# Kernel optimization log

Hardware: AMD Instinct MI355X
Metric: run time of the kernel (lower is better)

## Reference

```python
import jax, jax.numpy as jnp
import numpy as np

WCNT = 100000; EMB = 300; T = 256; S = 256; K = 10; L = 128; N = 8192


def gru_cell(x, h, wih, whh, bih, bhh):
    # torch GRU cell: gates ordered (r, z, n)
    gi = x @ wih.T + bih
    gh = h @ whh.T + bhh
    ir, iz, inn = jnp.split(gi, 3, axis=-1)
    hr, hz, hn = jnp.split(gh, 3, axis=-1)
    r = jax.nn.sigmoid(ir + hr)
    z = jax.nn.sigmoid(iz + hz)
    n = jnp.tanh(inn + r * hn)
    return (1.0 - z) * n + z * h


def gru_scan(xs, h0, wih, whh, bih, bhh):
    def step(h, x):
        hn = gru_cell(x, h, wih, whh, bih, bhh)
        return hn, hn
    _, ys = jax.lax.scan(step, h0, xs)
    return ys


def setup_inputs() -> dict:
    key = jax.random.key(0)
    ks = jax.random.split(key, 30)
    def rn(k, shape, scale=0.05):
        return jax.random.normal(k, shape, dtype=jnp.float32) * scale
    inp = {}
    inp["topic"] = jax.random.randint(ks[0], (L,), 0, WCNT)
    inp["score"] = jax.random.uniform(ks[1], (1,), dtype=jnp.float32)
    inp["time"] = jax.random.uniform(ks[2], (1,), dtype=jnp.float32)
    inp["h"] = rn(ks[3], (1, 1, S), 1.0)
    inp["vs"] = rn(ks[4], (N, T), 1.0)
    inp["hs"] = rn(ks[5], (N, 1, S), 1.0)
    inp["emb"] = rn(ks[6], (WCNT, EMB), 1.0)
    # word-level bidirectional GRU (input EMB, hidden T)
    inp["w_ih_f"] = rn(ks[7], (3 * T, EMB)); inp["w_hh_f"] = rn(ks[8], (3 * T, T))
    inp["b_ih_f"] = rn(ks[9], (3 * T,));     inp["b_hh_f"] = rn(ks[10], (3 * T,))
    inp["w_ih_b"] = rn(ks[11], (3 * T, EMB)); inp["w_hh_b"] = rn(ks[12], (3 * T, T))
    inp["b_ih_b"] = rn(ks[13], (3 * T,));     inp["b_hh_b"] = rn(ks[14], (3 * T,))
    # output GRU (input 2T, hidden T)
    inp["w_ih_o"] = rn(ks[15], (3 * T, 2 * T)); inp["w_hh_o"] = rn(ks[16], (3 * T, T))
    inp["b_ih_o"] = rn(ks[17], (3 * T,));       inp["b_hh_o"] = rn(ks[18], (3 * T,))
    # sequence GRU step (input 2T+1 for score_mode='double', hidden S)
    inp["w_ih_s"] = rn(ks[19], (3 * S, 2 * T + 1)); inp["w_hh_s"] = rn(ks[20], (3 * S, S))
    inp["b_ih_s"] = rn(ks[21], (3 * S,));           inp["b_hh_s"] = rn(ks[22], (3 * S,))
    # score head: in_features = topic_size + (2*S + 1) since with_last=True
    inp["score_w"] = rn(ks[23], (1, T + 2 * S + 1)); inp["score_b"] = rn(ks[24], (1,))
    return inp


def reference(topic, score, time, h, vs, hs, emb,
              w_ih_f, w_hh_f, b_ih_f, b_hh_f,
              w_ih_b, w_hh_b, b_ih_b, b_hh_b,
              w_ih_o, w_hh_o, b_ih_o, b_hh_o,
              w_ih_s, w_hh_s, b_ih_s, b_hh_s,
              score_w, score_b):
    # ---- TopicRNNModel (batch 1, batch dim dropped) ----
    x = emb[topic]                                  # [L, EMB]
    z0 = jnp.zeros((T,), dtype=x.dtype)
    yf = gru_scan(x, z0, w_ih_f, w_hh_f, b_ih_f, b_hh_f)          # [L, T]
    yb = gru_scan(x[::-1], z0, w_ih_b, w_hh_b, b_ih_b, b_hh_b)[::-1]
    y = jnp.concatenate([yf, yb], axis=-1)          # [L, 2T]
    v = gru_scan(y, z0, w_ih_o, w_hh_o, b_ih_o, b_hh_o)[-1]       # [T] = topic_v[0]
    # ---- AttnSeqModel: top-k attention over past hidden states ----
    alpha = vs @ v                                  # [N]
    a, idx = jax.lax.top_k(alpha, K)
    w = jax.nn.softmax(a)                           # [K]
    attn_h = w @ hs.reshape(-1, S)[idx]             # [S]
    length = jnp.full((1,), float(K), dtype=v.dtype)
    pred_v = jnp.concatenate([v, attn_h, h.reshape(-1), length])  # [T+2S+1]
    sc = (pred_v @ score_w.T + score_b).reshape(1, 1)
    # ---- GRU step (score_mode='double') ----
    gp = (score >= 0.5).astype(v.dtype)
    gn = (score < 0.5).astype(v.dtype)
    x_in = jnp.concatenate([v * gp, v * gn, score])  # [2T+1]
    h_new = gru_cell(x_in, h.reshape(-1), w_ih_s, w_hh_s, b_ih_s, b_hh_s).reshape(1, 1, S)
    # ---- updated history caches ----
    vs_new = jnp.concatenate([vs, v[None]], axis=0)
    hs_new = jnp.concatenate([hs, h_new], axis=0)
    return sc, h_new, vs_new, hs_new
```

## Files before the change

kernel.cpp:

```cpp
#include <hip/hip_runtime.h>
#include <cfloat>

#define EMB 300
#define TT 256
#define SS 256
#define KK 10
#define LL 128
#define NN 8192
#define G3 768

typedef _Float16 half2_t __attribute__((ext_vector_type(2)));

#if __has_builtin(__builtin_amdgcn_fdot2)
#define FDOT2(a, b, c) __builtin_amdgcn_fdot2((a), (b), (c), false)
#else
#define FDOT2(a, b, c) ((c) + (float)(a).x * (float)(b).x + (float)(a).y * (float)(b).y)
#endif

__device__ __forceinline__ float sigmoidf_(float x) {
    return __builtin_amdgcn_rcpf(1.0f + __expf(-x));
}
__device__ __forceinline__ float tanhf_(float x) {
    return 2.0f * __builtin_amdgcn_rcpf(1.0f + __expf(-2.0f * x)) - 1.0f;
}

__global__ void k_input_gates_word(const int* __restrict__ topic, const float* __restrict__ emb,
                                   const float* __restrict__ wihF, const float* __restrict__ bihF,
                                   const float* __restrict__ wihB, const float* __restrict__ bihB,
                                   float* __restrict__ giF, float* __restrict__ giB) {
    __shared__ float4 xl[EMB / 4];
    const int l = blockIdx.x;
    const int dir = blockIdx.y;
    const float* wih = dir ? wihB : wihF;
    const float* bih = dir ? bihB : bihF;
    float* gi = dir ? giB : giF;
    const int word = topic[l];
    const float4* xrow = (const float4*)(emb + (size_t)word * EMB);
    if (threadIdx.x < EMB / 4) xl[threadIdx.x] = xrow[threadIdx.x];
    __syncthreads();
    const int j = threadIdx.x;
    const float4* wr = (const float4*)(wih + (size_t)j * EMB);
    float acc = bih[j];
    #pragma unroll 5
    for (int c = 0; c < EMB / 4; ++c) {
        float4 w4 = wr[c], x4 = xl[c];
        acc += w4.x * x4.x + w4.y * x4.y + w4.z * x4.z + w4.w * x4.w;
    }
    gi[l * G3 + j] = acc;
}

__global__ void k_input_gates_out(const float* __restrict__ yF, const float* __restrict__ yB,
                                  const float* __restrict__ wihO, const float* __restrict__ bihO,
                                  float* __restrict__ giO) {
    __shared__ float4 yl[128];
    const int l = blockIdx.x;
    if (threadIdx.x < 64) {
        yl[threadIdx.x] = ((const float4*)(yF + l * TT))[threadIdx.x];
        yl[64 + threadIdx.x] = ((const float4*)(yB + l * TT))[threadIdx.x];
    }
    __syncthreads();
    const int j = threadIdx.x;
    const float4* wr = (const float4*)(wihO + (size_t)j * 512);
    float acc = bihO[j];
    #pragma unroll 4
    for (int c = 0; c < 128; ++c) {
        float4 w4 = wr[c], x4 = yl[c];
        acc += w4.x * x4.x + w4.y * x4.y + w4.z * x4.z + w4.w * x4.w;
    }
    giO[l * G3 + j] = acc;
}

__launch_bounds__(512, 2)
__global__ void k_gru_scan(const float* __restrict__ giA, const float* __restrict__ whhA,
                           const float* __restrict__ bhhA, float* __restrict__ yA, int revA,
                           const float* __restrict__ giB_, const float* __restrict__ whhB,
                           const float* __restrict__ bhhB, float* __restrict__ yB_, int revB) {
    const float* gi; const float* whh; const float* bhh; float* y; int rev;
    if (blockIdx.x == 0) { gi = giA; whh = whhA; bhh = bhhA; y = yA; rev = revA; }
    else                 { gi = giB_; whh = whhB; bhh = bhhB; y = yB_; rev = revB; }

    __shared__ __align__(16) unsigned int h_u32[TT / 2];
    __shared__ float part1[G3];
    __shared__ float gh_lds[G3];

    const int tid = threadIdx.x;
    const int grp = tid >> 8;
    const int r3 = tid & 255;
    const int row0 = r3 * 3;
    const int koff = grp * 128;

    half2_t w[3][64];
    float bias[3];
    #pragma unroll
    for (int rr = 0; rr < 3; ++rr) {
        const float4* wrow4 = (const float4*)(whh + (size_t)(row0 + rr) * TT + koff);
        #pragma unroll
        for (int q = 0; q < 32; ++q) {
            float4 f = wrow4[q];
            half2_t t0; t0.x = (_Float16)f.x; t0.y = (_Float16)f.y;
            half2_t t1; t1.x = (_Float16)f.z; t1.y = (_Float16)f.w;
            w[rr][2 * q] = t0;
            w[rr][2 * q + 1] = t1;
        }
        bias[rr] = (grp == 0) ? bhh[row0 + rr] : 0.0f;
    }

    for (int i = tid; i < TT / 2; i += blockDim.x) h_u32[i] = 0u;
    float hcur = 0.0f;
    __syncthreads();

    for (int t = 0; t < LL; ++t) {
        const int idx = rev ? (LL - 1 - t) : t;
        float gir = 0.f, giz = 0.f, gin = 0.f;
        if (grp == 0) {
            gir = gi[idx * G3 + r3];
            giz = gi[idx * G3 + 256 + r3];
            gin = gi[idx * G3 + 512 + r3];
        }
        float acc0 = bias[0], acc1 = bias[1], acc2 = bias[2];
        const uint4* h4 = (const uint4*)h_u32;
        #pragma unroll
        for (int c = 0; c < 16; ++c) {
            uint4 hu = h4[grp * 16 + c];
            half2_t hq0 = __builtin_bit_cast(half2_t, hu.x);
            half2_t hq1 = __builtin_bit_cast(half2_t, hu.y);
            half2_t hq2 = __builtin_bit_cast(half2_t, hu.z);
            half2_t hq3 = __builtin_bit_cast(half2_t, hu.w);
            acc0 = FDOT2(w[0][c * 4 + 0], hq0, acc0);
            acc1 = FDOT2(w[1][c * 4 + 0], hq0, acc1);
            acc2 = FDOT2(w[2][c * 4 + 0], hq0, acc2);
            acc0 = FDOT2(w[0][c * 4 + 1], hq1, acc0);
            acc1 = FDOT2(w[1][c * 4 + 1], hq1, acc1);
            acc2 = FDOT2(w[2][c * 4 + 1], hq1, acc2);
            acc0 = FDOT2(w[0][c * 4 + 2], hq2, acc0);
            acc1 = FDOT2(w[1][c * 4 + 2], hq2, acc1);
            acc2 = FDOT2(w[2][c * 4 + 2], hq2, acc2);
            acc0 = FDOT2(w[0][c * 4 + 3], hq3, acc0);
            acc1 = FDOT2(w[1][c * 4 + 3], hq3, acc1);
            acc2 = FDOT2(w[2][c * 4 + 3], hq3, acc2);
        }
        if (grp == 1) {
            part1[row0] = acc0; part1[row0 + 1] = acc1; part1[row0 + 2] = acc2;
        }
        __syncthreads();
        if (grp == 0) {
            gh_lds[row0]     = acc0 + part1[row0];
            gh_lds[row0 + 1] = acc1 + part1[row0 + 1];
            gh_lds[row0 + 2] = acc2 + part1[row0 + 2];
        }
        __syncthreads();
        if (grp == 0) {
            const int i = r3;
            float r = sigmoidf_(gir + gh_lds[i]);
            float z = sigmoidf_(giz + gh_lds[256 + i]);
            float n = tanhf_(gin + r * gh_lds[512 + i]);
            hcur = (1.0f - z) * n + z * hcur;
            y[idx * TT + i] = hcur;
            ((_Float16*)h_u32)[i] = (_Float16)hcur;
        }
        __syncthreads();
    }
}

__global__ void k_alpha(const float* __restrict__ vs, const float* __restrict__ v,
                        float* __restrict__ alpha) {
    const int wv = threadIdx.x >> 6;
    const int lane = threadIdx.x & 63;
    const int n = blockIdx.x * 4 + wv;
    float4 a = ((const float4*)(vs + (size_t)n * TT))[lane];
    float4 b = ((const float4*)v)[lane];
    float p = a.x * b.x + a.y * b.y + a.z * b.z + a.w * b.w;
    #pragma unroll
    for (int off = 32; off; off >>= 1) p += __shfl_down(p, off, 64);
    if (lane == 0) alpha[n] = p;
}

__global__ void k_gates_s(const float* __restrict__ v, const float* __restrict__ score,
                          const float* __restrict__ hin,
                          const float* __restrict__ wihS, const float* __restrict__ bihS,
                          const float* __restrict__ whhS, const float* __restrict__ bhhS,
                          float* __restrict__ gis, float* __restrict__ ghs) {
    const int j = blockIdx.x * blockDim.x + threadIdx.x;
    if (j >= G3) return;
    const float sc = score[0];
    const float gp = (sc >= 0.5f) ? 1.0f : 0.0f;
    const float gn = 1.0f - gp;
    const float* wi = wihS + (size_t)j * (2 * TT + 1);
    float a = bihS[j];
    for (int c = 0; c < TT; ++c) a += wi[c] * (v[c] * gp);
    for (int c = 0; c < TT; ++c) a += wi[TT + c] * (v[c] * gn);
    a += wi[2 * TT] * sc;
    gis[j] = a;
    const float* wh = whhS + (size_t)j * SS;
    float g = bhhS[j];
    for (int c = 0; c < SS; ++c) g += wh[c] * hin[c];
    ghs[j] = g;
}

__global__ void k_head(const float* __restrict__ alpha_g, const float* __restrict__ v,
                       const float* __restrict__ hin, const float* __restrict__ hs,
                       const float* __restrict__ score_w, const float* __restrict__ score_b,
                       const float* __restrict__ gis, const float* __restrict__ ghs,
                       float* __restrict__ d_out, float* __restrict__ hnew_ws) {
    __shared__ float sa[NN];
    __shared__ float wbv[16];
    __shared__ int wbi[16];
    __shared__ float topv[KK];
    __shared__ int topi[KK];
    __shared__ float wk[KK];
    __shared__ float predv[G3 + 8];
    const int tid = threadIdx.x;
    for (int i = tid; i < NN; i += 1024) sa[i] = alpha_g[i];
    __syncthreads();
    for (int it = 0; it < KK; ++it) {
        float bv = -FLT_MAX; int bi = 0x7fffffff;
        #pragma unroll
        for (int k = 0; k < 8; ++k) {
            int i = tid + 1024 * k;
            float x = sa[i];
            if (x > bv) { bv = x; bi = i; }
        }
        #pragma unroll
        for (int off = 32; off; off >>= 1) {
            float ov = __shfl_down(bv, off, 64);
            int oi = __shfl_down(bi, off, 64);
            if (ov > bv || (ov == bv && oi < bi)) { bv = ov; bi = oi; }
        }
        const int lane = tid & 63, wv = tid >> 6;
        if (lane == 0) { wbv[wv] = bv; wbi[wv] = bi; }
        __syncthreads();
        if (tid == 0) {
            float Bv = wbv[0]; int Bi = wbi[0];
            for (int wq = 1; wq < 16; ++wq)
                if (wbv[wq] > Bv || (wbv[wq] == Bv && wbi[wq] < Bi)) { Bv = wbv[wq]; Bi = wbi[wq]; }
            topv[it] = Bv; topi[it] = Bi;
            sa[Bi] = -FLT_MAX;
        }
        __syncthreads();
    }
    if (tid == 0) {
        float m = topv[0], s = 0.0f, e[KK];
        for (int k = 0; k < KK; ++k) { e[k] = __expf(topv[k] - m); s += e[k]; }
        float rs = 1.0f / s;
        for (int k = 0; k < KK; ++k) wk[k] = e[k] * rs;
    }
    __syncthreads();
    if (tid < TT) {
        float ah = 0.0f;
        #pragma unroll
        for (int k = 0; k < KK; ++k) ah += wk[k] * hs[(size_t)topi[k] * SS + tid];
        predv[tid] = v[tid];
        predv[TT + tid] = ah;
        predv[2 * TT + tid] = hin[tid];
        if (tid == 0) predv[G3] = (float)KK;
    }
    __syncthreads();
    if (tid < 64) {
        float p = 0.0f;
        for (int c = tid; c < G3 + 1; c += 64) p += predv[c] * score_w[c];
        #pragma unroll
        for (int off = 32; off; off >>= 1) p += __shfl_down(p, off, 64);
        if (tid == 0) d_out[0] = p + score_b[0];
    }
    if (tid < SS) {
        const int i = tid;
        float r = sigmoidf_(gis[i] + ghs[i]);
        float z = sigmoidf_(gis[TT + i] + ghs[TT + i]);
        float n = tanhf_(gis[2 * TT + i] + r * ghs[2 * TT + i]);
        float hn = (1.0f - z) * n + z * hin[i];
        d_out[1 + i] = hn;
        hnew_ws[i] = hn;
    }
}

__global__ void k_finalize(const float* __restrict__ vs, const float* __restrict__ hs,
                           const float* __restrict__ v, const float* __restrict__ hnew,
                           float* __restrict__ d_out) {
    const size_t i = (size_t)blockIdx.x * blockDim.x + threadIdx.x;
    const size_t stride = (size_t)gridDim.x * blockDim.x;
    float* vs_out = d_out + 1 + TT;
    float* hs_out = vs_out + (size_t)(NN + 1) * TT;
    for (size_t x = i; x < (size_t)NN * TT; x += stride) vs_out[x] = vs[x];
    for (size_t x = i; x < (size_t)NN * SS; x += stride) hs_out[x] = hs[x];
    if (i < TT) vs_out[(size_t)NN * TT + i] = v[i];
    if (i < SS) hs_out[(size_t)NN * SS + i] = hnew[i];
}

extern "C" void kernel_launch(void* const* d_in, const int* in_sizes, int n_in,
                              void* d_out, int out_size, void* d_ws, size_t ws_size,
                              hipStream_t stream) {
    (void)in_sizes; (void)n_in; (void)out_size; (void)ws_size;
    const int* topic = (const int*)d_in[0];
    const float* score = (const float*)d_in[1];
    const float* hin = (const float*)d_in[3];
    const float* vs = (const float*)d_in[4];
    const float* hs = (const float*)d_in[5];
    const float* emb = (const float*)d_in[6];
    const float* wihF = (const float*)d_in[7];
    const float* whhF = (const float*)d_in[8];
    const float* bihF = (const float*)d_in[9];
    const float* bhhF = (const float*)d_in[10];
    const float* wihB = (const float*)d_in[11];
    const float* whhB = (const float*)d_in[12];
    const float* bihB = (const float*)d_in[13];
    const float* bhhB = (const float*)d_in[14];
    const float* wihO = (const float*)d_in[15];
    const float* whhO = (const float*)d_in[16];
    const float* bihO = (const float*)d_in[17];
    const float* bhhO = (const float*)d_in[18];
    const float* wihS = (const float*)d_in[19];
    const float* whhS = (const float*)d_in[20];
    const float* bihS = (const float*)d_in[21];
    const float* bhhS = (const float*)d_in[22];
    const float* scw = (const float*)d_in[23];
    const float* scb = (const float*)d_in[24];

    float* ws = (float*)d_ws;
    float* giF = ws;
    float* giB = giF + LL * G3;
    float* yF  = giB + LL * G3;
    float* yB  = yF + LL * TT;
    float* giO = yB + LL * TT;
    float* yO  = giO + LL * G3;
    float* alpha = yO + LL * TT;
    float* gis = alpha + NN;
    float* ghs = gis + G3;
    float* hnew = ghs + G3;
    float* out = (float*)d_out;
    const float* v = yO + 127 * TT;

    k_input_gates_word<<<dim3(LL, 2), G3, 0, stream>>>(topic, emb, wihF, bihF, wihB, bihB, giF, giB);
    k_gru_scan<<<2, 512, 0, stream>>>(giF, whhF, bhhF, yF, 0, giB, whhB, bhhB, yB, 1);
    k_input_gates_out<<<LL, G3, 0, stream>>>(yF, yB, wihO, bihO, giO);
    k_gru_scan<<<1, 512, 0, stream>>>(giO, whhO, bhhO, yO, 0, giO, whhO, bhhO, yO, 0);
    k_alpha<<<NN / 4, 256, 0, stream>>>(vs, v, alpha);
    k_gates_s<<<6, 128, 0, stream>>>(v, score, hin, wihS, bihS, whhS, bhhS, gis, ghs);
    k_head<<<1, 1024, 0, stream>>>(alpha, v, hin, hs, scw, scb, gis, ghs, out, hnew);
    k_finalize<<<2048, 256, 0, stream>>>(vs, hs, v, hnew, out);
}
```

Baseline: 754.2 us.

## Prepack recurrent weights to fp16 per-thread layout, drop a barrier, parallelize gates_s

```diff
diff --git a/kernel.cpp b/kernel.cpp
--- a/kernel.cpp
+++ b/kernel.cpp
@@ -8,6 +8,7 @@
 #define LL 128
 #define NN 8192
 #define G3 768
+#define PKN (512 * 192)
 
 typedef _Float16 half2_t __attribute__((ext_vector_type(2)));
 
@@ -22,6 +23,29 @@
 }
 __device__ __forceinline__ float tanhf_(float x) {
     return 2.0f * __builtin_amdgcn_rcpf(1.0f + __expf(-2.0f * x)) - 1.0f;
+}
+
+__global__ void k_pack(const float* __restrict__ whhF, const float* __restrict__ whhB,
+                       const float* __restrict__ whhO, unsigned int* __restrict__ pF,
+                       unsigned int* __restrict__ pB, unsigned int* __restrict__ pO) {
+    const int m = blockIdx.y;
+    const float* src = m == 0 ? whhF : (m == 1 ? whhB : whhO);
+    unsigned int* dst = m == 0 ? pF : (m == 1 ? pB : pO);
+    const int g = blockIdx.x * 1024 + threadIdx.x;
+    const int tid_s = g / 192;
+    const int idx = g - tid_s * 192;
+    const int rr = idx >> 6;
+    const int c = (idx >> 2) & 15;
+    const int q = idx & 3;
+    const int grp = tid_s >> 8;
+    const int r3 = tid_s & 255;
+    const int row = rr * 256 + r3;
+    const int kb = grp * 128 + c * 8 + q * 2;
+    const float e0 = src[row * 256 + kb];
+    const float e1 = src[row * 256 + kb + 1];
+    unsigned int lo = (unsigned int)__builtin_bit_cast(unsigned short, (_Float16)e0);
+    unsigned int hi = (unsigned int)__builtin_bit_cast(unsigned short, (_Float16)e1);
+    dst[g] = lo | (hi << 16);
 }
 
 __global__ void k_input_gates_word(const int* __restrict__ topic, const float* __restrict__ emb,
@@ -71,41 +95,34 @@
 }
 
 __launch_bounds__(512, 2)
-__global__ void k_gru_scan(const float* __restrict__ giA, const float* __restrict__ whhA,
+__global__ void k_gru_scan(const float* __restrict__ giA, const unsigned int* __restrict__ pA,
                            const float* __restrict__ bhhA, float* __restrict__ yA, int revA,
-                           const float* __restrict__ giB_, const float* __restrict__ whhB,
+                           const float* __restrict__ giB_, const unsigned int* __restrict__ pB,
                            const float* __restrict__ bhhB, float* __restrict__ yB_, int revB) {
-    const float* gi; const float* whh; const float* bhh; float* y; int rev;
-    if (blockIdx.x == 0) { gi = giA; whh = whhA; bhh = bhhA; y = yA; rev = revA; }
-    else                 { gi = giB_; whh = whhB; bhh = bhhB; y = yB_; rev = revB; }
+    const float* gi; const unsigned int* pk; const float* bhh; float* y; int rev;
+    if (blockIdx.x == 0) { gi = giA;  pk = pA; bhh = bhhA; y = yA;  rev = revA; }
+    else                 { gi = giB_; pk = pB; bhh = bhhB; y = yB_; rev = revB; }
 
     __shared__ __align__(16) unsigned int h_u32[TT / 2];
-    __shared__ float part1[G3];
-    __shared__ float gh_lds[G3];
+    __shared__ float part[G3];
 
     const int tid = threadIdx.x;
     const int grp = tid >> 8;
     const int r3 = tid & 255;
-    const int row0 = r3 * 3;
-    const int koff = grp * 128;
-
-    half2_t w[3][64];
-    float bias[3];
-    #pragma unroll
-    for (int rr = 0; rr < 3; ++rr) {
-        const float4* wrow4 = (const float4*)(whh + (size_t)(row0 + rr) * TT + koff);
-        #pragma unroll
-        for (int q = 0; q < 32; ++q) {
-            float4 f = wrow4[q];
-            half2_t t0; t0.x = (_Float16)f.x; t0.y = (_Float16)f.y;
-            half2_t t1; t1.x = (_Float16)f.z; t1.y = (_Float16)f.w;
-            w[rr][2 * q] = t0;
-            w[rr][2 * q + 1] = t1;
-        }
-        bias[rr] = (grp == 0) ? bhh[row0 + rr] : 0.0f;
-    }
-
-    for (int i = tid; i < TT / 2; i += blockDim.x) h_u32[i] = 0u;
+
+    const uint4* wp = (const uint4*)(pk + (size_t)tid * 192);
+    uint4 wa[16], wb[16], wc[16];
+    #pragma unroll
+    for (int i = 0; i < 16; ++i) wa[i] = wp[i];
+    #pragma unroll
+    for (int i = 0; i < 16; ++i) wb[i] = wp[16 + i];
+    #pragma unroll
+    for (int i = 0; i < 16; ++i) wc[i] = wp[32 + i];
+
+    float bias0 = 0.f, bias1 = 0.f, bias2 = 0.f;
+    if (grp == 0) { bias0 = bhh[r3]; bias1 = bhh[256 + r3]; bias2 = bhh[512 + r3]; }
+
+    for (int i = tid; i < TT / 2; i += 512) h_u32[i] = 0u;
     float hcur = 0.0f;
     __syncthreads();
 
@@ -117,46 +134,39 @@
             giz = gi[idx * G3 + 256 + r3];
             gin = gi[idx * G3 + 512 + r3];
         }
-        float acc0 = bias[0], acc1 = bias[1], acc2 = bias[2];
-        const uint4* h4 = (const uint4*)h_u32;
+        float acc0 = bias0, acc1 = bias1, acc2 = bias2;
+        const uint4* h4 = ((const uint4*)h_u32) + grp * 16;
         #pragma unroll
         for (int c = 0; c < 16; ++c) {
-            uint4 hu = h4[grp * 16 + c];
-            half2_t hq0 = __builtin_bit_cast(half2_t, hu.x);
-            half2_t hq1 = __builtin_bit_cast(half2_t, hu.y);
-            half2_t hq2 = __builtin_bit_cast(half2_t, hu.z);
-            half2_t hq3 = __builtin_bit_cast(half2_t, hu.w);
-            acc0 = FDOT2(w[0][c * 4 + 0], hq0, acc0);
-            acc1 = FDOT2(w[1][c * 4 + 0], hq0, acc1);
-            acc2 = FDOT2(w[2][c * 4 + 0], hq0, acc2);
-            acc0 = FDOT2(w[0][c * 4 + 1], hq1, acc0);
-            acc1 = FDOT2(w[1][c * 4 + 1], hq1, acc1);
-            acc2 = FDOT2(w[2][c * 4 + 1], hq1, acc2);
-            acc0 = FDOT2(w[0][c * 4 + 2], hq2, acc0);
-            acc1 = FDOT2(w[1][c * 4 + 2], hq2, acc1);
-            acc2 = FDOT2(w[2][c * 4 + 2], hq2, acc2);
-            acc0 = FDOT2(w[0][c * 4 + 3], hq3, acc0);
-            acc1 = FDOT2(w[1][c * 4 + 3], hq3, acc1);
-            acc2 = FDOT2(w[2][c * 4 + 3], hq3, acc2);
+            uint4 hu = h4[c];
+            half2_t h0 = __builtin_bit_cast(half2_t, hu.x);
+            half2_t h1 = __builtin_bit_cast(half2_t, hu.y);
+            half2_t h2 = __builtin_bit_cast(half2_t, hu.z);
+            half2_t h3 = __builtin_bit_cast(half2_t, hu.w);
+            acc0 = FDOT2(__builtin_bit_cast(half2_t, wa[c].x), h0, acc0);
+            acc1 = FDOT2(__builtin_bit_cast(half2_t, wb[c].x), h0, acc1);
+            acc2 = FDOT2(__builtin_bit_cast(half2_t, wc[c].x), h0, acc2);
+            acc0 = FDOT2(__builtin_bit_cast(half2_t, wa[c].y), h1, acc0);
+            acc1 = FDOT2(__builtin_bit_cast(half2_t, wb[c].y), h1, acc1);
+            acc2 = FDOT2(__builtin_bit_cast(half2_t, wc[c].y), h1, acc2);
+            acc0 = FDOT2(__builtin_bit_cast(half2_t, wa[c].z), h2, acc0);
+            acc1 = FDOT2(__builtin_bit_cast(half2_t, wb[c].z), h2, acc1);
+            acc2 = FDOT2(__builtin_bit_cast(half2_t, wc[c].z), h2, acc2);
+            acc0 = FDOT2(__builtin_bit_cast(half2_t, wa[c].w), h3, acc0);
+            acc1 = FDOT2(__builtin_bit_cast(half2_t, wb[c].w), h3, acc1);
+            acc2 = FDOT2(__builtin_bit_cast(half2_t, wc[c].w), h3, acc2);
         }
         if (grp == 1) {
-            part1[row0] = acc0; part1[row0 + 1] = acc1; part1[row0 + 2] = acc2;
+            part[r3] = acc0; part[256 + r3] = acc1; part[512 + r3] = acc2;
         }
         __syncthreads();
         if (grp == 0) {
-            gh_lds[row0]     = acc0 + part1[row0];
-            gh_lds[row0 + 1] = acc1 + part1[row0 + 1];
-            gh_lds[row0 + 2] = acc2 + part1[row0 + 2];
-        }
-        __syncthreads();
-        if (grp == 0) {
-            const int i = r3;
-            float r = sigmoidf_(gir + gh_lds[i]);
-            float z = sigmoidf_(giz + gh_lds[256 + i]);
-            float n = tanhf_(gin + r * gh_lds[512 + i]);
+            float r = sigmoidf_(gir + acc0 + part[r3]);
+            float z = sigmoidf_(giz + acc1 + part[256 + r3]);
+            float n = tanhf_(gin + r * (acc2 + part[512 + r3]));
             hcur = (1.0f - z) * n + z * hcur;
-            y[idx * TT + i] = hcur;
-            ((_Float16*)h_u32)[i] = (_Float16)hcur;
+            y[idx * TT + r3] = hcur;
+            ((_Float16*)h_u32)[r3] = (_Float16)hcur;
         }
         __syncthreads();
     }
@@ -180,21 +190,34 @@
                           const float* __restrict__ wihS, const float* __restrict__ bihS,
                           const float* __restrict__ whhS, const float* __restrict__ bhhS,
                           float* __restrict__ gis, float* __restrict__ ghs) {
-    const int j = blockIdx.x * blockDim.x + threadIdx.x;
+    const int j = (blockIdx.x * blockDim.x + threadIdx.x) >> 6;
+    const int lane = threadIdx.x & 63;
     if (j >= G3) return;
     const float sc = score[0];
     const float gp = (sc >= 0.5f) ? 1.0f : 0.0f;
     const float gn = 1.0f - gp;
     const float* wi = wihS + (size_t)j * (2 * TT + 1);
-    float a = bihS[j];
-    for (int c = 0; c < TT; ++c) a += wi[c] * (v[c] * gp);
-    for (int c = 0; c < TT; ++c) a += wi[TT + c] * (v[c] * gn);
-    a += wi[2 * TT] * sc;
-    gis[j] = a;
+    float a = 0.0f;
+    #pragma unroll
+    for (int k = 0; k < 8; ++k) {
+        int c = lane + 64 * k;
+        float x = (c < 256) ? v[c] * gp : v[c - 256] * gn;
+        a += wi[c] * x;
+    }
+    if (lane == 0) a += wi[2 * TT] * sc;
     const float* wh = whhS + (size_t)j * SS;
-    float g = bhhS[j];
-    for (int c = 0; c < SS; ++c) g += wh[c] * hin[c];
-    ghs[j] = g;
+    float g = 0.0f;
+    #pragma unroll
+    for (int k = 0; k < 4; ++k) {
+        int c = lane + 64 * k;
+        g += wh[c] * hin[c];
+    }
+    #pragma unroll
+    for (int off = 32; off; off >>= 1) {
+        a += __shfl_down(a, off, 64);
+        g += __shfl_down(g, off, 64);
+    }
+    if (lane == 0) { gis[j] = a + bihS[j]; ghs[j] = g + bhhS[j]; }
 }
 
 __global__ void k_head(const float* __restrict__ alpha_g, const float* __restrict__ v,
@@ -326,15 +349,19 @@
     float* gis = alpha + NN;
     float* ghs = gis + G3;
     float* hnew = ghs + G3;
+    unsigned int* pF = (unsigned int*)(hnew + TT);
+    unsigned int* pB = pF + PKN;
+    unsigned int* pO = pB + PKN;
     float* out = (float*)d_out;
     const float* v = yO + 127 * TT;
 
+    k_pack<<<dim3(96, 3), 1024, 0, stream>>>(whhF, whhB, whhO, pF, pB, pO);
     k_input_gates_word<<<dim3(LL, 2), G3, 0, stream>>>(topic, emb, wihF, bihF, wihB, bihB, giF, giB);
-    k_gru_scan<<<2, 512, 0, stream>>>(giF, whhF, bhhF, yF, 0, giB, whhB, bhhB, yB, 1);
+    k_gru_scan<<<2, 512, 0, stream>>>(giF, pF, bhhF, yF, 0, giB, pB, bhhB, yB, 1);
     k_input_gates_out<<<LL, G3, 0, stream>>>(yF, yB, wihO, bihO, giO);
-    k_gru_scan<<<1, 512, 0, stream>>>(giO, whhO, bhhO, yO, 0, giO, whhO, bhhO, yO, 0);
+    k_gru_scan<<<1, 512, 0, stream>>>(giO, pO, bhhO, yO, 0, giO, pO, bhhO, yO, 0);
     k_alpha<<<NN / 4, 256, 0, stream>>>(vs, v, alpha);
-    k_gates_s<<<6, 128, 0, stream>>>(v, score, hin, wihS, bihS, whhS, bhhS, gis, ghs);
+    k_gates_s<<<G3 / 4, 256, 0, stream>>>(v, score, hin, wihS, bihS, whhS, bhhS, gis, ghs);
     k_head<<<1, 1024, 0, stream>>>(alpha, v, hin, hs, scw, scb, gis, ghs, out, hnew);
     k_finalize<<<2048, 256, 0, stream>>>(vs, hs, v, hnew, out);
 }
```

Measured after the change: 622.4 us. -17.5%, faster.
